# Kernel optimization log

Hardware: AMD Instinct MI355X
Metric: run time of the kernel (lower is better)

The kernel has to match this reference:

```python
import math
import jax, jax.numpy as jnp
import numpy as np

N = 2048
HID = 1024
ALPHA = 0.5
BETA = 0.1  # greedy term is zero when coords is None


def setup_inputs() -> dict:
    key = jax.random.key(0)
    k1, k2, k3, k4 = jax.random.split(key, 4)
    node_emb = jax.random.normal(k1, (N, HID), jnp.float32)
    demands = jax.random.uniform(k2, (N,), jnp.float32)  # each < 1 << capacity
    # query_net: Linear(hid+2 -> hid); key_net: Linear(hid -> hid)
    Wq = jax.random.normal(k3, (HID, HID + 2), jnp.float32) / math.sqrt(HID + 2)
    bq = jnp.zeros((HID,), jnp.float32)
    Wk = jax.random.normal(k4, (HID, HID), jnp.float32) / math.sqrt(HID)
    bk = jnp.zeros((HID,), jnp.float32)
    return {"node_emb": node_emb, "demands": demands, "Wq": Wq, "bq": bq,
            "Wk": Wk, "bk": bk, "capacity": 40, "depot_idx": 0}


def _decode(node_emb, demands, Wq, bq, Wk, bk, capacity, depot_idx):
    n, h = node_emb.shape
    cap = jnp.float32(capacity)
    inv_sqrt = 1.0 / math.sqrt(h)
    # key_net is a per-node linear map: precompute once (same math as per-step gather+linear)
    K = node_emb @ Wk.T + bk  # [N, H]
    idx = jnp.arange(n)
    # demands < 1, capacity = 40 => >= 39 customers per route => few depot returns;
    # T = N + N//8 safely bounds customer picks + route-closing depot emissions.
    T = n + n // 8
    visited0 = jnp.zeros((n,), bool).at[depot_idx].set(True)

    def step(carry, _):
        visited, load, last, done = carry
        feasible = (~visited) & (demands <= load)
        has_cand = jnp.any(feasible)
        # context = [emb(last), load/capacity, avgd]; avgd = 0 since coords is None
        ctx = jnp.concatenate([node_emb[last],
                               jnp.stack([load / cap, jnp.float32(0.0)])])
        q = Wq @ ctx + bq                      # [H]
        s = ALPHA * ((K @ q) * inv_sqrt)       # [N] scores over all nodes
        s_m = jnp.where(feasible, s, -jnp.inf)
        cand = jnp.argmax(s_m)
        take = has_cand & (~done)
        nxt = jnp.where(take, cand, depot_idx).astype(jnp.int32)
        step_score = jnp.where(take, s[cand], jnp.float32(0.0))
        visited = visited | ((idx == cand) & take)
        load = jnp.where(take, load - demands[cand], cap)  # route end resets load
        done = done | ((~take) & jnp.all(visited))
        return (visited, load, nxt, done), (nxt, step_score)

    carry0 = (visited0, cap, jnp.int32(depot_idx), jnp.bool_(False))
    _, (seq, scores) = jax.lax.scan(step, carry0, None, length=T)
    tour = jnp.concatenate([jnp.array([depot_idx], seq.dtype), seq])  # [T+1]
    return tour, scores


def reference(node_emb, demands, Wq, bq, Wk, bk, capacity, depot_idx):
    # tour: flat visitation order; routes are the segments between depot occurrences
    # (trailing depots are padding once all customers are served).
    # scores: selected decoder score at each step (0 at depot/padding steps).
    return _decode(node_emb, demands, Wq, bq, Wk, bk, capacity, depot_idx)
```

## Files before the change

### kernel.cpp

```cpp
#include <hip/hip_runtime.h>
#include <hip/hip_bf16.h>


#define NN 2048
#define HH 1024
#define TSTEPS (NN + NN / 8)
#define TILE 64
#define KT 16
#define KCAND 128
#define KL 15

__global__ __launch_bounds__(256) void prep_wqh(const float* __restrict__ Wq,
                                                float* __restrict__ Wqh) {
  int id = blockIdx.x * 256 + threadIdx.x;
  int r = id >> 10, c = id & 1023;
  Wqh[id] = Wq[r * (HH + 2) + c];
}

__global__ __launch_bounds__(256) void gemm_nt(const float* __restrict__ A, int lda,
                                               const float* __restrict__ B, int ldb,
                                               float* __restrict__ C, int ldc,
                                               int K, const float* __restrict__ bias) {
  __shared__ float As[KT][TILE + 4];
  __shared__ float Bs[KT][TILE + 4];
  const int i0 = blockIdx.y * TILE;
  const int j0 = blockIdx.x * TILE;
  const int t = threadIdx.x;
  const int srow = t >> 2, sq = t & 3;
  const int tx = t & 15, ty = t >> 4;
  float acc[4][4] = {};
  for (int k0 = 0; k0 < K; k0 += KT) {
    float4 av = *(const float4*)&A[(size_t)(i0 + srow) * lda + k0 + sq * 4];
    float4 bv = *(const float4*)&B[(size_t)(j0 + srow) * ldb + k0 + sq * 4];
    __syncthreads();
    As[sq * 4 + 0][srow] = av.x; As[sq * 4 + 1][srow] = av.y;
    As[sq * 4 + 2][srow] = av.z; As[sq * 4 + 3][srow] = av.w;
    Bs[sq * 4 + 0][srow] = bv.x; Bs[sq * 4 + 1][srow] = bv.y;
    Bs[sq * 4 + 2][srow] = bv.z; Bs[sq * 4 + 3][srow] = bv.w;
    __syncthreads();
#pragma unroll
    for (int k = 0; k < KT; ++k) {
      float4 a4 = *(const float4*)&As[k][ty * 4];
      float4 b4 = *(const float4*)&Bs[k][tx * 4];
      float a[4] = {a4.x, a4.y, a4.z, a4.w};
      float b[4] = {b4.x, b4.y, b4.z, b4.w};
#pragma unroll
      for (int m = 0; m < 4; ++m)
#pragma unroll
        for (int n = 0; n < 4; ++n) acc[m][n] = fmaf(a[m], b[n], acc[m][n]);
    }
  }
  float bb[4] = {0.f, 0.f, 0.f, 0.f};
  if (bias) {
#pragma unroll
    for (int n = 0; n < 4; ++n) bb[n] = bias[j0 + tx * 4 + n];
  }
#pragma unroll
  for (int m = 0; m < 4; ++m) {
    float4 st = {acc[m][0] + bb[0], acc[m][1] + bb[1], acc[m][2] + bb[2], acc[m][3] + bb[3]};
    *(float4*)&C[(size_t)(i0 + ty * 4 + m) * ldc + j0 + tx * 4] = st;
  }
}

__global__ __launch_bounds__(64) void uv_k(const float* __restrict__ Kmat,
                                           const float* __restrict__ Wq,
                                           const float* __restrict__ bq,
                                           float* __restrict__ u, float* __restrict__ v) {
  int i = blockIdx.x;
  int lane = threadIdx.x;
  float su = 0.f, sv = 0.f;
#pragma unroll
  for (int m = 0; m < HH / 64; ++m) {
    int j = lane + 64 * m;
    float kv = Kmat[(size_t)i * HH + j];
    su = fmaf(kv, Wq[(size_t)j * (HH + 2) + HH], su);
    sv = fmaf(kv, bq[j], sv);
  }
#pragma unroll
  for (int off = 32; off; off >>= 1) {
    su += __shfl_down(su, off, 64);
    sv += __shfl_down(sv, off, 64);
  }
  if (lane == 0) { u[i] = su; v[i] = sv; }
}

__device__ __forceinline__ unsigned f2key(float f) {
  unsigned x = __float_as_uint(f);
  return x ^ ((x >> 31) ? 0xFFFFFFFFu : 0x80000000u);
}
__device__ __forceinline__ float key2f(unsigned k) {
  unsigned x = (k & 0x80000000u) ? (k ^ 0x80000000u) : ~k;
  return __uint_as_float(x);
}
__device__ __forceinline__ unsigned ub16(float x) {
  unsigned b = __float_as_uint(x);
  if (x > 0.f && (b & 0xFFFFu)) b += 0x10000u;
  return b >> 16;
}
__global__ __launch_bounds__(256) void prep_cand(const float* __restrict__ GT,
                                                 const float* __restrict__ u,
                                                 uint2* __restrict__ cand,
                                                 unsigned* __restrict__ pc16,
                                                 uint2* __restrict__ thrpk2) {
  __shared__ float rowv[NN];
  __shared__ float su_[NN];
  __shared__ int hist[256];
  __shared__ float red15[256];
  __shared__ float red128[256];
  __shared__ unsigned c128k[KCAND];
  __shared__ int c128i[KCAND];
  __shared__ unsigned char markA[NN];
  __shared__ unsigned char markB[NN];
  __shared__ int s_d, s_need, s_gt, s_eq, s_gt2, s_eq2, s_flag;
  const int row = blockIdx.x, t = threadIdx.x;
  for (int i = t; i < NN; i += 256) {
    rowv[i] = GT[(size_t)row * NN + i];
    su_[i] = u[i];
    markA[i] = 0;
    markB[i] = 0;
  }
  __syncthreads();
  unsigned prefix = 0;
  int need = KCAND;
  for (int pass = 0; pass < 4; ++pass) {
    hist[t] = 0;
    __syncthreads();
    const int shift = 24 - 8 * pass;
    for (int i = t; i < NN; i += 256) {
      unsigned k = f2key(rowv[i]);
      if (pass == 0 || (k >> (shift + 8)) == (prefix >> (shift + 8)))
        atomicAdd(&hist[(k >> shift) & 0xFF], 1);
    }
    __syncthreads();
    if (t == 0) {
      int cum = 0, d = 255;
      for (; d > 0; --d) {
        if (cum + hist[d] >= need) break;
        cum += hist[d];
      }
      s_d = d;
      s_need = need - cum;
    }
    __syncthreads();
    prefix |= ((unsigned)s_d) << shift;
    need = s_need;
    __syncthreads();
  }
  const unsigned thrk = prefix;
  if (t == 0) { s_gt = 0; s_eq = 0; }
  __syncthreads();
  for (int i = t; i < NN; i += 256) {
    unsigned k = f2key(rowv[i]);
    if (k > thrk) {
      int p = atomicAdd(&s_gt, 1);
      cand[(size_t)row * KCAND + p] = make_uint2(__float_as_uint(rowv[i]), (unsigned)i);
      c128k[p] = k;
      c128i[p] = i;
      markA[i] = 1;
    }
  }
  __syncthreads();
  const int cgt = s_gt;
  for (int i = t; i < NN; i += 256) {
    if (f2key(rowv[i]) == thrk) {
      int p = atomicAdd(&s_eq, 1);
      if (p < KCAND - cgt) {
        cand[(size_t)row * KCAND + cgt + p] = make_uint2(__float_as_uint(rowv[i]), (unsigned)i);
        c128k[cgt + p] = thrk;
        c128i[cgt + p] = i;
        markA[i] = 1;
      }
    }
  }
  __syncthreads();
  unsigned pfx2 = 0;
  need = KL;
  for (int pass = 0; pass < 4; ++pass) {
    hist[t] = 0;
    __syncthreads();
    const int shift = 24 - 8 * pass;
    for (int i = t; i < KCAND; i += 256) {
      unsigned k = c128k[i];
      if (pass == 0 || (k >> (shift + 8)) == (pfx2 >> (shift + 8)))
        atomicAdd(&hist[(k >> shift) & 0xFF], 1);
    }
    __syncthreads();
    if (t == 0) {
      int cum = 0, d = 255;
      for (; d > 0; --d) {
        if (cum + hist[d] >= need) break;
        cum += hist[d];
      }
      s_d = d;
      s_need = need - cum;
    }
    __syncthreads();
    pfx2 |= ((unsigned)s_d) << shift;
    need = s_need;
    __syncthreads();
  }
  const unsigned thrk15 = pfx2;
  if (t == 0) { s_gt2 = 0; s_eq2 = 0; s_flag = 0; }
  __syncthreads();
  for (int i = t; i < KCAND; i += 256) {
    if (c128k[i] > thrk15) {
      int p = atomicAdd(&s_gt2, 1);
      pc16[(size_t)row * KL + p] = (c128k[i] & 0xFFFFF800u) | (unsigned)c128i[i];
      markB[c128i[i]] = 1;
      if (fabsf(key2f(c128k[i])) + fabsf(su_[c128i[i]]) >= 128.0f) s_flag = 1;
    }
  }
  __syncthreads();
  const int cgt2 = s_gt2;
  for (int i = t; i < KCAND; i += 256) {
    if (c128k[i] == thrk15) {
      int p = atomicAdd(&s_eq2, 1);
      if (p < KL - cgt2) {
        pc16[(size_t)row * KL + cgt2 + p] = (thrk15 & 0xFFFFF800u) | (unsigned)c128i[i];
        markB[c128i[i]] = 1;
        if (fabsf(key2f(thrk15)) + fabsf(su_[c128i[i]]) >= 128.0f) s_flag = 1;
      }
    }
  }
  if (t == 0 && fabsf(key2f(thrk15)) >= 128.0f) s_flag = 1;
  __syncthreads();
  float lm15 = -__builtin_inff(), lm128 = -__builtin_inff();
  for (int i = t; i < NN; i += 256) {
    float gu = rowv[i] + su_[i];
    if (!markB[i]) lm15 = fmaxf(lm15, gu);
    if (!markA[i]) lm128 = fmaxf(lm128, gu);
  }
  red15[t] = lm15;
  red128[t] = lm128;
  __syncthreads();
  for (int s = 128; s; s >>= 1) {
    if (t < s) {
      red15[t] = fmaxf(red15[t], red15[t + s]);
      red128[t] = fmaxf(red128[t], red128[t + s]);
    }
    __syncthreads();
  }
  if (t == 0) {
    const float INF = __builtin_inff();
    float t15 = s_flag ? INF : key2f(thrk15);
    float m15 = s_flag ? INF : red15[0];
    thrpk2[row] = make_uint2((ub16(t15) << 16) | ub16(m15),
                             (ub16(key2f(thrk)) << 16) | ub16(red128[0]));
  }
}

__global__ __launch_bounds__(256) void warm_k(const float* __restrict__ a, int n,
                                              float* __restrict__ sink) {
  float s = 0.f;
  const float4* a4 = (const float4*)a;
  for (int i = threadIdx.x; i < n / 4; i += 256) {
    float4 x = a4[i];
    s += x.x + x.y + x.z + x.w;
  }
  if (s == 1.2345e-30f) sink[blockIdx.x] = s;
}

#define DPP_MERGE2(CTRL)                                                      \
  {                                                                           \
    int ovb = __builtin_amdgcn_update_dpp(                                    \
        (int)0xFF800000, __float_as_int(bv), (CTRL), 0xf, 0xf, false);        \
    int oib = __builtin_amdgcn_update_dpp(                                    \
        0x7fffffff, bi, (CTRL), 0xf, 0xf, false);                             \
    float ov = __int_as_float(ovb);                                           \
    if (ov > bv || (ov == bv && oib < bi)) { bv = ov; bi = oib; }             \
  }

#define KRED(CTRL)                                                            \
  {                                                                           \
    unsigned o1 = (unsigned)__builtin_amdgcn_update_dpp(                      \
        0, (int)m1, (CTRL), 0xf, 0xf, false);                                 \
    unsigned o2 = (unsigned)__builtin_amdgcn_update_dpp(                      \
        0, (int)m2, (CTRL), 0xf, 0xf, false);                                 \
    unsigned mn = min(m1, o1);                                                \
    m1 = max(m1, o1);                                                         \
    m2 = max(max(m2, o2), mn);                                                \
  }

struct Pick { int take; int nxt; };

__device__ __noinline__ Pick tier3_scan(const float* __restrict__ GT,
                                        const float2* sdu, int row, int lane,
                                        float load, float lr, int depot) {
  const float NEGINF = -__builtin_inff();
  const float4* rowp = (const float4*)(GT + (size_t)row * NN);
  const float4* du4 = (const float4*)sdu;
  float fv = NEGINF;
  int fi = NN;
#pragma unroll
  for (int r = 0; r < 8; ++r) {
    float4 g4 = rowp[r * 64 + lane];
    float4 pA = du4[(r * 64 + lane) * 2];
    float4 pB = du4[(r * 64 + lane) * 2 + 1];
    float gl[4] = {g4.x, g4.y, g4.z, g4.w};
    float dl[4] = {pA.x, pA.z, pB.x, pB.z};
    float ul[4] = {pA.y, pA.w, pB.y, pB.w};
    float cv = NEGINF;
    int cj = 0;
#pragma unroll
    for (int j = 0; j < 4; ++j) {
      float tt = fmaf(ul[j], lr, gl[j]);
      bool feas = (dl[j] <= load);
      if (feas && tt > cv) { cv = tt; cj = j; }
    }
    if (cv > fv) { fv = cv; fi = 4 * (r * 64 + lane) + cj; }
  }
  float bv = fv;
  int bi = fi;
  DPP_MERGE2(0x111); DPP_MERGE2(0x112); DPP_MERGE2(0x114);
  DPP_MERGE2(0x118); DPP_MERGE2(0x142); DPP_MERGE2(0x143);
  float fbv = __int_as_float(__builtin_amdgcn_readlane(__float_as_int(bv), 63));
  int fbi = __builtin_amdgcn_readlane(bi, 63);
  Pick p;
  p.take = (fbv > NEGINF) ? 1 : 0;
  p.nxt = p.take ? fbi : depot;
  return p;
}

__global__ __launch_bounds__(64, 1) void decode(const float* __restrict__ GT,
                                                const uint2* __restrict__ cand,
                                                const unsigned* __restrict__ pc16,
                                                const uint2* __restrict__ thrpk2,
                                                const float* __restrict__ u,
                                                const float* __restrict__ demands,
                                                const int* __restrict__ capp,
                                                const int* __restrict__ depotp,
                                                float* __restrict__ lrbuf,
                                                float* __restrict__ out) {
  __shared__ __align__(16) unsigned s_pc[NN * KL + 64];
  __shared__ __align__(16) float2 s_du[NN];
  __shared__ __align__(16) uint2 s_thr[NN];
  __shared__ __align__(16) unsigned short s_tour[TSTEPS + 2];

  const int lane = threadIdx.x;
  const int depot = *depotp;
  const float capf = (float)(*capp);
  const float INF = __builtin_inff();
  const float C0 = 0.015625f;
  const float MARGIN = 0.5f;
  const float EGM = 0.0625f;
  float* sduf = (float*)s_du;

  for (int i = lane; i < NN; i += 64) {
    s_du[i] = make_float2(demands[i], u[i]);
    s_thr[i] = thrpk2[i];
  }
  {
    const uint4* p4 = (const uint4*)pc16;
    uint4* q4 = (uint4*)s_pc;
    for (int i = lane; i < NN * KL / 4; i += 64) q4[i] = p4[i];
  }
  if (lane == 0) {
    sduf[2 * depot] = INF;
    s_tour[0] = (unsigned short)depot;
  }

  int ntaken = 0, lasts = depot;
  float load = capf;
  float lr = load / capf;
  int step = 0;
  const int lcl = (lane < KL) ? lane : (KL - 1);

  for (; step < TSTEPS; ++step) {
    const int row = lasts;
    unsigned pw = s_pc[row * KL + lcl];
    uint2 pk2 = s_thr[row];
    int i1x = (int)(pw & 0x7FFu);
    float2 du1 = s_du[i1x];
    float g1 = key2f(pw & 0xFFFFF800u);
    float t1 = fmaf(du1.y, lr, g1);
    bool act = (lane < KL) && (du1.x <= load);
    unsigned m1 = act ? ((f2key(t1) & 0xFFFFF800u) | ((~(unsigned)i1x) & 0x7FFu)) : 0u;
    unsigned m2 = 0u;
    KRED(0x111); KRED(0x112); KRED(0x114); KRED(0x118);
    unsigned rv1k = (unsigned)__builtin_amdgcn_readlane((int)m1, 15);
    unsigned rv2k = (unsigned)__builtin_amdgcn_readlane((int)m2, 15);
    float rv1f = key2f(rv1k & 0xFFFFF800u);
    float rv2f = key2f(rv2k | 0x7FFu);
    float t15 = __uint_as_float(pk2.x & 0xFFFF0000u);
    float m15 = __uint_as_float(pk2.x << 16);
    float B1 = fmaf(1.0f - lr, t15, lr * m15) + MARGIN;
    int take, nxt;
    if (__builtin_expect((rv1f > B1) && (rv1f > rv2f + EGM), 1)) {
      take = 1;
      nxt = (int)((~rv1k) & 0x7FFu);
    } else {
      uint4 cc = ((const uint4*)(cand + (size_t)row * KCAND))[lane];
      float bv = -INF;
      int bi = 0x7fffffff;
      {
        float ga = __uint_as_float(cc.x); int ia = (int)cc.y;
        float gb = __uint_as_float(cc.z); int ib = (int)cc.w;
        float2 da = s_du[ia];
        float2 db = s_du[ib];
        float ta = fmaf(da.y, lr, ga);
        float tb = fmaf(db.y, lr, gb);
        if ((da.x <= load) && (ta > bv || (ta == bv && ia < bi))) { bv = ta; bi = ia; }
        if ((db.x <= load) && (tb > bv || (tb == bv && ib < bi))) { bv = tb; bi = ib; }
      }
      DPP_MERGE2(0x111); DPP_MERGE2(0x112); DPP_MERGE2(0x114);
      DPP_MERGE2(0x118); DPP_MERGE2(0x142); DPP_MERGE2(0x143);
      float rbv = __int_as_float(__builtin_amdgcn_readlane(__float_as_int(bv), 63));
      int rbi = __builtin_amdgcn_readlane(bi, 63);
      float t128 = __uint_as_float(pk2.y & 0xFFFF0000u);
      float m128 = __uint_as_float(pk2.y << 16);
      float B2 = fmaf(1.0f - lr, t128, lr * m128) + MARGIN;
      if (rbv > B2) {
        take = 1; nxt = rbi;
      } else {
        Pick p = tier3_scan(GT, (const float2*)s_du, row, lane, load, lr, depot);
        take = p.take; nxt = p.nxt;
      }
    }

    if (lane == 0) {
      s_tour[1 + step] = (unsigned short)nxt;
      lrbuf[step] = take ? lr : -1.0f;
    }
    if (take) {
      float dwin = s_du[nxt].x;
      load = load - dwin;
      ntaken++;
      if (lane == 0) sduf[2 * nxt] = INF;
    } else {
      load = capf;
      if (ntaken == NN - 1) { ++step; break; }
    }
    lasts = nxt;
    lr = load / capf;
  }

  for (int q = step + lane; q < TSTEPS; q += 64) {
    s_tour[1 + q] = (unsigned short)depot;
    lrbuf[q] = -1.0f;
  }
  asm volatile("s_waitcnt vmcnt(0)" ::: "memory");
  for (int i = lane; i <= TSTEPS; i += 64) out[i] = (float)s_tour[i];
  for (int s = lane; s < TSTEPS; s += 64) {
    float lrs = lrbuf[s];
    float sc = 0.0f;
    if (lrs >= 0.0f) {
      int lastI = (int)s_tour[s];
      int biI = (int)s_tour[s + 1];
      float g = GT[(size_t)lastI * NN + biI];
      sc = fmaf(s_du[biI].y, lrs, g) * C0;
    }
    out[1 + TSTEPS + s] = sc;
  }
}

extern "C" void kernel_launch(void* const* d_in, const int* in_sizes, int n_in,
                              void* d_out, int out_size, void* d_ws, size_t ws_size,
                              hipStream_t stream) {
  const float* emb     = (const float*)d_in[0];
  const float* demands = (const float*)d_in[1];
  const float* Wq      = (const float*)d_in[2];
  const float* bq      = (const float*)d_in[3];
  const float* Wk      = (const float*)d_in[4];
  const float* bk      = (const float*)d_in[5];
  const int* cap       = (const int*)d_in[6];
  const int* depot     = (const int*)d_in[7];
  float* out           = (float*)d_out;

  char* ws = (char*)d_ws;
  float* Kmat = (float*)(ws);
  float* Z    = (float*)(ws + ((size_t)8 << 20));
  float* GT   = (float*)(ws + ((size_t)16 << 20));
  float* Wqh  = (float*)(ws + ((size_t)32 << 20));
  float* u    = (float*)(ws + ((size_t)36 << 20));
  float* v    = (float*)(ws + ((size_t)36 << 20) + 8192);
  float* sink = (float*)(ws + ((size_t)36 << 20) + 32768);
  uint2* cnd  = (uint2*)Wqh;
  unsigned* pc16g = (unsigned*)(ws + ((size_t)34 << 20));
  uint2* thrpk2g  = (uint2*)(ws + ((size_t)34 << 20) + (128 << 10));
  float* lrbuf    = (float*)(ws + ((size_t)34 << 20) + (160 << 10));

  hipLaunchKernelGGL(prep_wqh, dim3(4096), dim3(256), 0, stream, Wq, Wqh);
  hipLaunchKernelGGL(gemm_nt, dim3(HH / TILE, NN / TILE), dim3(256), 0, stream,
                     emb, HH, Wk, HH, Kmat, HH, HH, bk);
  hipLaunchKernelGGL(gemm_nt, dim3(HH / TILE, NN / TILE), dim3(256), 0, stream,
                     emb, HH, Wqh, HH, Z, HH, HH, (const float*)nullptr);
  hipLaunchKernelGGL(uv_k, dim3(NN), dim3(64), 0, stream, Kmat, Wq, bq, u, v);
  hipLaunchKernelGGL(gemm_nt, dim3(NN / TILE, NN / TILE), dim3(256), 0, stream,
                     Z, HH, Kmat, HH, GT, NN, HH, v);
  hipLaunchKernelGGL(prep_cand, dim3(NN), dim3(256), 0, stream, GT, u, cnd,
                     pc16g, thrpk2g);
  hipLaunchKernelGGL(warm_k, dim3(128), dim3(256), 0, stream,
                     (const float*)cnd, NN * KCAND * 2 + (160 << 8), sink);
  hipLaunchKernelGGL(decode, dim3(1), dim3(64), 0, stream, GT, cnd,
                     pc16g, thrpk2g, u, demands, cap, depot, lrbuf, out);
}
```

Before: 1.837 ms.

## Switch to compact candidate-list decode once few customers remain

```diff
diff --git a/kernel.cpp b/kernel.cpp
--- a/kernel.cpp
+++ b/kernel.cpp
@@ -9,6 +9,7 @@
 #define KT 16
 #define KCAND 128
 #define KL 15
+#define CTRIG 128
 
 __global__ __launch_bounds__(256) void prep_wqh(const float* __restrict__ Wq,
                                                 float* __restrict__ Wqh) {
@@ -335,6 +336,8 @@
   __shared__ __align__(16) float2 s_du[NN];
   __shared__ __align__(16) uint2 s_thr[NN];
   __shared__ __align__(16) unsigned short s_tour[TSTEPS + 2];
+  __shared__ __align__(16) int s_cmp[CTRIG];
+  __shared__ int s_ccnt;
 
   const int lane = threadIdx.x;
   const int depot = *depotp;
@@ -359,7 +362,7 @@
     s_tour[0] = (unsigned short)depot;
   }
 
-  int ntaken = 0, lasts = depot;
+  int ntaken = 0, lasts = depot, done = 0;
   float load = capf;
   float lr = load / capf;
   int step = 0;
@@ -422,16 +425,81 @@
       lrbuf[step] = take ? lr : -1.0f;
     }
     if (take) {
-      float dwin = s_du[nxt].x;
+      unsigned long long mk = __ballot(i1x == nxt);
+      float dwin;
+      if (__builtin_expect(mk != 0ull, 1)) {
+        int wl = (int)(__ffsll(mk) - 1);
+        dwin = __shfl(du1.x, wl, 64);
+      } else {
+        dwin = s_du[nxt].x;
+      }
       load = load - dwin;
       ntaken++;
       if (lane == 0) sduf[2 * nxt] = INF;
     } else {
       load = capf;
-      if (ntaken == NN - 1) { ++step; break; }
+      if (ntaken == NN - 1) { done = 1; ++step; break; }
     }
     lasts = nxt;
     lr = load / capf;
+    if (NN - 1 - ntaken <= CTRIG) { ++step; break; }
+  }
+
+  if (!done && step < TSTEPS) {
+    if (lane == 0) s_ccnt = 0;
+    __syncthreads();
+    for (int i = lane; i < NN; i += 64) {
+      if (s_du[i].x < INF) {
+        int p = atomicAdd(&s_ccnt, 1);
+        s_cmp[p] = i;
+      }
+    }
+    __syncthreads();
+    const int cnt = s_ccnt;
+    int ci0 = (lane < cnt) ? s_cmp[lane] : -1;
+    int ci1 = (lane + 64 < cnt) ? s_cmp[lane + 64] : -1;
+    float cd0 = INF, cu0 = 0.f, cd1 = INF, cu1 = 0.f;
+    if (ci0 >= 0) { float2 t = s_du[ci0]; cd0 = t.x; cu0 = t.y; }
+    if (ci1 >= 0) { float2 t = s_du[ci1]; cd1 = t.x; cu1 = t.y; }
+
+    for (; step < TSTEPS; ++step) {
+      const float* rp = GT + (size_t)lasts * NN;
+      float g0 = 0.f, g1 = 0.f;
+      if (ci0 >= 0) g0 = rp[ci0];
+      if (ci1 >= 0) g1 = rp[ci1];
+      float bv = -INF;
+      int bi = 0x7fffffff;
+      if (ci0 >= 0 && cd0 <= load) { bv = fmaf(cu0, lr, g0); bi = ci0; }
+      if (ci1 >= 0 && cd1 <= load) {
+        float tv = fmaf(cu1, lr, g1);
+        if (tv > bv || (tv == bv && ci1 < bi)) { bv = tv; bi = ci1; }
+      }
+      DPP_MERGE2(0x111); DPP_MERGE2(0x112); DPP_MERGE2(0x114);
+      DPP_MERGE2(0x118); DPP_MERGE2(0x142); DPP_MERGE2(0x143);
+      float fbv = __int_as_float(__builtin_amdgcn_readlane(__float_as_int(bv), 63));
+      int fbi = __builtin_amdgcn_readlane(bi, 63);
+      int take = (fbv > -INF) ? 1 : 0;
+      int nxt = take ? fbi : depot;
+      if (lane == 0) {
+        s_tour[1 + step] = (unsigned short)nxt;
+        lrbuf[step] = take ? lr : -1.0f;
+      }
+      if (take) {
+        float dw = (ci0 == nxt) ? cd0 : cd1;
+        unsigned long long mk = __ballot((ci0 == nxt) || (ci1 == nxt));
+        int wl = (int)(__ffsll(mk) - 1);
+        float dwin = __shfl(dw, wl, 64);
+        load = load - dwin;
+        ntaken++;
+        if (ci0 == nxt) cd0 = INF;
+        if (ci1 == nxt) cd1 = INF;
+      } else {
+        load = capf;
+        if (ntaken == NN - 1) { ++step; break; }
+      }
+      lasts = nxt;
+      lr = load / capf;
+    }
   }
 
   for (int q = step + lane; q < TSTEPS; q += 64) {
```

Measured after the change: 1.888 ms. 2.8% more time.

## Shrink per-row top candidate list to 8 with packed demand and u

Applied to the files above, without the earlier changes.

```diff
diff --git a/kernel.cpp b/kernel.cpp
--- a/kernel.cpp
+++ b/kernel.cpp
@@ -8,7 +8,7 @@
 #define TILE 64
 #define KT 16
 #define KCAND 128
-#define KL 15
+#define KL8 8
 
 __global__ __launch_bounds__(256) void prep_wqh(const float* __restrict__ Wq,
                                                 float* __restrict__ Wqh) {
@@ -97,15 +97,23 @@
   if (x > 0.f && (b & 0xFFFFu)) b += 0x10000u;
   return b >> 16;
 }
+__device__ __forceinline__ unsigned bf16rne(float x) {
+  unsigned b = __float_as_uint(x);
+  b += 0x7FFFu + ((b >> 16) & 1u);
+  return b >> 16;
+}
+
 __global__ __launch_bounds__(256) void prep_cand(const float* __restrict__ GT,
                                                  const float* __restrict__ u,
+                                                 const float* __restrict__ demands,
                                                  uint2* __restrict__ cand,
-                                                 unsigned* __restrict__ pc16,
-                                                 uint2* __restrict__ thrpk2) {
+                                                 uint2* __restrict__ pc8,
+                                                 unsigned* __restrict__ thr8g,
+                                                 unsigned* __restrict__ thr2g) {
   __shared__ float rowv[NN];
   __shared__ float su_[NN];
   __shared__ int hist[256];
-  __shared__ float red15[256];
+  __shared__ float red8[256];
   __shared__ float red128[256];
   __shared__ unsigned c128k[KCAND];
   __shared__ int c128i[KCAND];
@@ -174,7 +182,7 @@
   }
   __syncthreads();
   unsigned pfx2 = 0;
-  need = KL;
+  need = KL8;
   for (int pass = 0; pass < 4; ++pass) {
     hist[t] = 0;
     __syncthreads();
@@ -199,53 +207,62 @@
     need = s_need;
     __syncthreads();
   }
-  const unsigned thrk15 = pfx2;
+  const unsigned thrk8 = pfx2;
   if (t == 0) { s_gt2 = 0; s_eq2 = 0; s_flag = 0; }
   __syncthreads();
   for (int i = t; i < KCAND; i += 256) {
-    if (c128k[i] > thrk15) {
+    if (c128k[i] > thrk8) {
       int p = atomicAdd(&s_gt2, 1);
-      pc16[(size_t)row * KL + p] = (c128k[i] & 0xFFFFF800u) | (unsigned)c128i[i];
-      markB[c128i[i]] = 1;
-      if (fabsf(key2f(c128k[i])) + fabsf(su_[c128i[i]]) >= 128.0f) s_flag = 1;
+      int idx = c128i[i];
+      float uu = su_[idx];
+      float dd = demands[idx];
+      pc8[(size_t)row * KL8 + p] =
+          make_uint2((bf16rne(uu) << 16) | ub16(dd),
+                     (c128k[i] & 0xFFFFF800u) | (unsigned)idx);
+      markB[idx] = 1;
+      if (fabsf(key2f(c128k[i])) >= 128.0f || fabsf(uu) >= 8.0f) s_flag = 1;
     }
   }
   __syncthreads();
   const int cgt2 = s_gt2;
   for (int i = t; i < KCAND; i += 256) {
-    if (c128k[i] == thrk15) {
+    if (c128k[i] == thrk8) {
       int p = atomicAdd(&s_eq2, 1);
-      if (p < KL - cgt2) {
-        pc16[(size_t)row * KL + cgt2 + p] = (thrk15 & 0xFFFFF800u) | (unsigned)c128i[i];
-        markB[c128i[i]] = 1;
-        if (fabsf(key2f(thrk15)) + fabsf(su_[c128i[i]]) >= 128.0f) s_flag = 1;
+      if (p < KL8 - cgt2) {
+        int idx = c128i[i];
+        float uu = su_[idx];
+        float dd = demands[idx];
+        pc8[(size_t)row * KL8 + cgt2 + p] =
+            make_uint2((bf16rne(uu) << 16) | ub16(dd),
+                       (thrk8 & 0xFFFFF800u) | (unsigned)idx);
+        markB[idx] = 1;
+        if (fabsf(key2f(thrk8)) >= 128.0f || fabsf(uu) >= 8.0f) s_flag = 1;
       }
     }
   }
-  if (t == 0 && fabsf(key2f(thrk15)) >= 128.0f) s_flag = 1;
-  __syncthreads();
-  float lm15 = -__builtin_inff(), lm128 = -__builtin_inff();
+  __syncthreads();
+  float lm8 = -__builtin_inff(), lm128 = -__builtin_inff();
   for (int i = t; i < NN; i += 256) {
     float gu = rowv[i] + su_[i];
-    if (!markB[i]) lm15 = fmaxf(lm15, gu);
+    if (!markB[i]) lm8 = fmaxf(lm8, gu);
     if (!markA[i]) lm128 = fmaxf(lm128, gu);
   }
-  red15[t] = lm15;
+  red8[t] = lm8;
   red128[t] = lm128;
   __syncthreads();
   for (int s = 128; s; s >>= 1) {
     if (t < s) {
-      red15[t] = fmaxf(red15[t], red15[t + s]);
+      red8[t] = fmaxf(red8[t], red8[t + s]);
       red128[t] = fmaxf(red128[t], red128[t + s]);
     }
     __syncthreads();
   }
   if (t == 0) {
     const float INF = __builtin_inff();
-    float t15 = s_flag ? INF : key2f(thrk15);
-    float m15 = s_flag ? INF : red15[0];
-    thrpk2[row] = make_uint2((ub16(t15) << 16) | ub16(m15),
-                             (ub16(key2f(thrk)) << 16) | ub16(red128[0]));
+    float t8 = s_flag ? INF : key2f(thrk8);
+    float m8 = s_flag ? INF : red8[0];
+    thr8g[row] = (ub16(t8) << 16) | ub16(m8);
+    thr2g[row] = (ub16(key2f(thrk)) << 16) | ub16(red128[0]);
   }
 }
 
@@ -323,17 +340,18 @@
 
 __global__ __launch_bounds__(64, 1) void decode(const float* __restrict__ GT,
                                                 const uint2* __restrict__ cand,
-                                                const unsigned* __restrict__ pc16,
-                                                const uint2* __restrict__ thrpk2,
+                                                const uint2* __restrict__ pc8,
+                                                const unsigned* __restrict__ thr8g,
+                                                const unsigned* __restrict__ thr2g,
                                                 const float* __restrict__ u,
                                                 const float* __restrict__ demands,
                                                 const int* __restrict__ capp,
                                                 const int* __restrict__ depotp,
                                                 float* __restrict__ lrbuf,
                                                 float* __restrict__ out) {
-  __shared__ __align__(16) unsigned s_pc[NN * KL + 64];
+  __shared__ __align__(16) uint2 s_pc8[NN * KL8];
   __shared__ __align__(16) float2 s_du[NN];
-  __shared__ __align__(16) uint2 s_thr[NN];
+  __shared__ __align__(16) unsigned s_thr[NN];
   __shared__ __align__(16) unsigned short s_tour[TSTEPS + 2];
 
   const int lane = threadIdx.x;
@@ -342,54 +360,64 @@
   const float INF = __builtin_inff();
   const float C0 = 0.015625f;
   const float MARGIN = 0.5f;
-  const float EGM = 0.0625f;
+  const float EGM = 0.25f;
   float* sduf = (float*)s_du;
 
   for (int i = lane; i < NN; i += 64) {
     s_du[i] = make_float2(demands[i], u[i]);
-    s_thr[i] = thrpk2[i];
+    s_thr[i] = thr8g[i];
   }
   {
-    const uint4* p4 = (const uint4*)pc16;
-    uint4* q4 = (uint4*)s_pc;
-    for (int i = lane; i < NN * KL / 4; i += 64) q4[i] = p4[i];
+    const uint4* p4 = (const uint4*)pc8;
+    uint4* q4 = (uint4*)s_pc8;
+    for (int i = lane; i < NN * KL8 / 2; i += 64) q4[i] = p4[i];
   }
   if (lane == 0) {
     sduf[2 * depot] = INF;
     s_tour[0] = (unsigned short)depot;
   }
+  unsigned vmask = 0u;
+  if (lane == (depot >> 5)) vmask |= 1u << (depot & 31);
 
   int ntaken = 0, lasts = depot;
   float load = capf;
   float lr = load / capf;
   int step = 0;
-  const int lcl = (lane < KL) ? lane : (KL - 1);
+  const int lcl8 = (lane < KL8) ? lane : (KL8 - 1);
 
   for (; step < TSTEPS; ++step) {
     const int row = lasts;
-    unsigned pw = s_pc[row * KL + lcl];
-    uint2 pk2 = s_thr[row];
-    int i1x = (int)(pw & 0x7FFu);
-    float2 du1 = s_du[i1x];
-    float g1 = key2f(pw & 0xFFFFF800u);
-    float t1 = fmaf(du1.y, lr, g1);
-    bool act = (lane < KL) && (du1.x <= load);
-    unsigned m1 = act ? ((f2key(t1) & 0xFFFFF800u) | ((~(unsigned)i1x) & 0x7FFu)) : 0u;
+    uint2 e = s_pc8[(row << 3) + lcl8];
+    unsigned pk = s_thr[row];
+    int i1x = (int)(e.y & 0x7FFu);
+    float g1 = key2f(e.y & 0xFFFFF800u);
+    float u1 = __uint_as_float(e.x & 0xFFFF0000u);
+    unsigned dhb = e.x << 16;
+    float dh = __uint_as_float(dhb);
+    float dl = __uint_as_float(dhb - 0x00010000u);
+    float t1 = fmaf(u1, lr, g1);
+    bool poss = (lane < KL8) && (dl < load);
+    unsigned m1 = poss ? ((f2key(t1) & 0xFFFFF800u) | ((~(unsigned)i1x) & 0x7FFu)) : 0u;
     unsigned m2 = 0u;
-    KRED(0x111); KRED(0x112); KRED(0x114); KRED(0x118);
-    unsigned rv1k = (unsigned)__builtin_amdgcn_readlane((int)m1, 15);
-    unsigned rv2k = (unsigned)__builtin_amdgcn_readlane((int)m2, 15);
+    KRED(0x111); KRED(0x112); KRED(0x114);
+    unsigned rv1k = (unsigned)__builtin_amdgcn_readlane((int)m1, 7);
+    unsigned rv2k = (unsigned)__builtin_amdgcn_readlane((int)m2, 7);
     float rv1f = key2f(rv1k & 0xFFFFF800u);
     float rv2f = key2f(rv2k | 0x7FFu);
-    float t15 = __uint_as_float(pk2.x & 0xFFFF0000u);
-    float m15 = __uint_as_float(pk2.x << 16);
-    float B1 = fmaf(1.0f - lr, t15, lr * m15) + MARGIN;
+    int wid = (int)((~rv1k) & 0x7FFu);
+    float t8 = __uint_as_float(pk & 0xFFFF0000u);
+    float m8 = __uint_as_float(pk << 16);
+    float B1 = fmaf(1.0f - lr, t8, lr * m8) + MARGIN;
+    unsigned long long okb = __ballot((lane < KL8) && (i1x == wid) && (dh <= load));
+    unsigned long long visb = __ballot((lane == (wid >> 5)) && ((vmask >> (wid & 31)) & 1u));
     int take, nxt;
-    if (__builtin_expect((rv1f > B1) && (rv1f > rv2f + EGM), 1)) {
+    if (__builtin_expect((rv1f > B1) && (rv1f > rv2f + EGM) &&
+                         (okb != 0ull) && (visb == 0ull), 1)) {
       take = 1;
-      nxt = (int)((~rv1k) & 0x7FFu);
+      nxt = wid;
     } else {
       uint4 cc = ((const uint4*)(cand + (size_t)row * KCAND))[lane];
+      unsigned pk2 = thr2g[row];
       float bv = -INF;
       int bi = 0x7fffffff;
       {
@@ -406,8 +434,8 @@
       DPP_MERGE2(0x118); DPP_MERGE2(0x142); DPP_MERGE2(0x143);
       float rbv = __int_as_float(__builtin_amdgcn_readlane(__float_as_int(bv), 63));
       int rbi = __builtin_amdgcn_readlane(bi, 63);
-      float t128 = __uint_as_float(pk2.y & 0xFFFF0000u);
-      float m128 = __uint_as_float(pk2.y << 16);
+      float t128 = __uint_as_float(pk2 & 0xFFFF0000u);
+      float m128 = __uint_as_float(pk2 << 16);
       float B2 = fmaf(1.0f - lr, t128, lr * m128) + MARGIN;
       if (rbv > B2) {
         take = 1; nxt = rbi;
@@ -426,6 +454,7 @@
       load = load - dwin;
       ntaken++;
       if (lane == 0) sduf[2 * nxt] = INF;
+      if (lane == (nxt >> 5)) vmask |= 1u << (nxt & 31);
     } else {
       load = capf;
       if (ntaken == NN - 1) { ++step; break; }
@@ -474,10 +503,11 @@
   float* u    = (float*)(ws + ((size_t)36 << 20));
   float* v    = (float*)(ws + ((size_t)36 << 20) + 8192);
   float* sink = (float*)(ws + ((size_t)36 << 20) + 32768);
-  uint2* cnd  = (uint2*)Wqh;
-  unsigned* pc16g = (unsigned*)(ws + ((size_t)34 << 20));
-  uint2* thrpk2g  = (uint2*)(ws + ((size_t)34 << 20) + (128 << 10));
-  float* lrbuf    = (float*)(ws + ((size_t)34 << 20) + (160 << 10));
+  uint2* cnd      = (uint2*)Wqh;
+  uint2* pc8g     = (uint2*)(ws + ((size_t)34 << 20));
+  unsigned* thr8g = (unsigned*)(ws + ((size_t)34 << 20) + (128 << 10));
+  unsigned* thr2g = (unsigned*)(ws + ((size_t)34 << 20) + (136 << 10));
+  float* lrbuf    = (float*)(ws + ((size_t)34 << 20) + (144 << 10));
 
   hipLaunchKernelGGL(prep_wqh, dim3(4096), dim3(256), 0, stream, Wq, Wqh);
   hipLaunchKernelGGL(gemm_nt, dim3(HH / TILE, NN / TILE), dim3(256), 0, stream,
@@ -487,10 +517,10 @@
   hipLaunchKernelGGL(uv_k, dim3(NN), dim3(64), 0, stream, Kmat, Wq, bq, u, v);
   hipLaunchKernelGGL(gemm_nt, dim3(NN / TILE, NN / TILE), dim3(256), 0, stream,
                      Z, HH, Kmat, HH, GT, NN, HH, v);
-  hipLaunchKernelGGL(prep_cand, dim3(NN), dim3(256), 0, stream, GT, u, cnd,
-                     pc16g, thrpk2g);
+  hipLaunchKernelGGL(prep_cand, dim3(NN), dim3(256), 0, stream, GT, u, demands,
+                     cnd, pc8g, thr8g, thr2g);
   hipLaunchKernelGGL(warm_k, dim3(128), dim3(256), 0, stream,
                      (const float*)cnd, NN * KCAND * 2 + (160 << 8), sink);
   hipLaunchKernelGGL(decode, dim3(1), dim3(64), 0, stream, GT, cnd,
-                     pc16g, thrpk2g, u, demands, cap, depot, lrbuf, out);
-}
+                     pc8g, thr8g, thr2g, u, demands, cap, depot, lrbuf, out);
+}
```

Result: slower. 2.230 ms (+21.4%).

## Add helper wavefront to prefetch candidate rows into LDS for decode

Applied to the files above, without the earlier changes.

```diff
diff --git a/kernel.cpp b/kernel.cpp
--- a/kernel.cpp
+++ b/kernel.cpp
@@ -321,22 +321,26 @@
   return p;
 }
 
-__global__ __launch_bounds__(64, 1) void decode(const float* __restrict__ GT,
-                                                const uint2* __restrict__ cand,
-                                                const unsigned* __restrict__ pc16,
-                                                const uint2* __restrict__ thrpk2,
-                                                const float* __restrict__ u,
-                                                const float* __restrict__ demands,
-                                                const int* __restrict__ capp,
-                                                const int* __restrict__ depotp,
-                                                float* __restrict__ lrbuf,
-                                                float* __restrict__ out) {
+__global__ __launch_bounds__(128, 1) void decode(const float* __restrict__ GT,
+                                                 const uint2* __restrict__ cand,
+                                                 const unsigned* __restrict__ pc16,
+                                                 const uint2* __restrict__ thrpk2,
+                                                 const float* __restrict__ u,
+                                                 const float* __restrict__ demands,
+                                                 const int* __restrict__ capp,
+                                                 const int* __restrict__ depotp,
+                                                 float* __restrict__ lrbuf,
+                                                 float* __restrict__ out) {
   __shared__ __align__(16) unsigned s_pc[NN * KL + 64];
   __shared__ __align__(16) float2 s_du[NN];
   __shared__ __align__(16) uint2 s_thr[NN];
   __shared__ __align__(16) unsigned short s_tour[TSTEPS + 2];
-
-  const int lane = threadIdx.x;
+  __shared__ __align__(16) uint4 s_stage[64];
+  __shared__ volatile int s_req;
+  __shared__ volatile int s_ack;
+
+  const int tid = threadIdx.x;
+  const int lane = tid & 63;
   const int depot = *depotp;
   const float capf = (float)(*capp);
   const float INF = __builtin_inff();
@@ -345,18 +349,37 @@
   const float EGM = 0.0625f;
   float* sduf = (float*)s_du;
 
-  for (int i = lane; i < NN; i += 64) {
+  for (int i = tid; i < NN; i += 128) {
     s_du[i] = make_float2(demands[i], u[i]);
     s_thr[i] = thrpk2[i];
   }
   {
     const uint4* p4 = (const uint4*)pc16;
     uint4* q4 = (uint4*)s_pc;
-    for (int i = lane; i < NN * KL / 4; i += 64) q4[i] = p4[i];
-  }
-  if (lane == 0) {
+    for (int i = tid; i < NN * KL / 4; i += 128) q4[i] = p4[i];
+  }
+  if (tid == 0) {
     sduf[2 * depot] = INF;
     s_tour[0] = (unsigned short)depot;
+    s_req = 0;
+    s_ack = 0;
+  }
+  __syncthreads();
+
+  if (tid >= 64) {
+    int last = 0;
+    for (;;) {
+      int rq = s_req;
+      if (rq == last) continue;
+      if (rq == -1) return;
+      last = rq;
+      int row = rq & (NN - 1);
+      uint4 c = ((const uint4*)(cand + (size_t)row * KCAND))[lane];
+      s_stage[lane] = c;
+      asm volatile("s_waitcnt lgkmcnt(0)" ::: "memory");
+      __builtin_amdgcn_sched_barrier(0);
+      s_ack = rq;
+    }
   }
 
   int ntaken = 0, lasts = depot;
@@ -367,6 +390,8 @@
 
   for (; step < TSTEPS; ++step) {
     const int row = lasts;
+    const int seq = ((step + 1) << 11) | row;
+    if (lane == 0) s_req = seq;
     unsigned pw = s_pc[row * KL + lcl];
     uint2 pk2 = s_thr[row];
     int i1x = (int)(pw & 0x7FFu);
@@ -389,7 +414,19 @@
       take = 1;
       nxt = (int)((~rv1k) & 0x7FFu);
     } else {
-      uint4 cc = ((const uint4*)(cand + (size_t)row * KCAND))[lane];
+      uint4 cc;
+      int got = 0;
+#pragma unroll 1
+      for (int z = 0; z < 6; ++z) {
+        if (s_ack == seq) { got = 1; break; }
+      }
+      if (got) {
+        asm volatile("s_waitcnt lgkmcnt(0)" ::: "memory");
+        __builtin_amdgcn_sched_barrier(0);
+        cc = s_stage[lane];
+      } else {
+        cc = ((const uint4*)(cand + (size_t)row * KCAND))[lane];
+      }
       float bv = -INF;
       int bi = 0x7fffffff;
       {
@@ -434,6 +471,8 @@
     lr = load / capf;
   }
 
+  if (lane == 0) s_req = -1;
+
   for (int q = step + lane; q < TSTEPS; q += 64) {
     s_tour[1 + q] = (unsigned short)depot;
     lrbuf[q] = -1.0f;
@@ -491,6 +530,6 @@
                      pc16g, thrpk2g);
   hipLaunchKernelGGL(warm_k, dim3(128), dim3(256), 0, stream,
                      (const float*)cnd, NN * KCAND * 2 + (160 << 8), sink);
-  hipLaunchKernelGGL(decode, dim3(1), dim3(64), 0, stream, GT, cnd,
+  hipLaunchKernelGGL(decode, dim3(1), dim3(128), 0, stream, GT, cnd,
                      pc16g, thrpk2g, u, demands, cap, depot, lrbuf, out);
 }
```

Measured after the change: 1.956 ms. 1.06x slower.
